# Kernel tuning notes

Measured on AMD Instinct MI355X. Metric: run time of the kernel, lower is better.

The kernel has to match this reference:

```python
import jax, jax.numpy as jnp
import numpy as np

DIM = 256
NUM_LAYERS = 64


def setup_inputs() -> dict:
    key = jax.random.key(0)
    kx, kt = jax.random.split(key)
    x = jax.random.normal(kx, (32768, DIM), dtype=jnp.float32)
    # theta[l, p]: scalar angle for pair p in layer l. Odd-offset layers use only
    # the first DIM//2 - 1 entries. Matches torch.randn(()) * pi init.
    theta = jax.random.normal(kt, (NUM_LAYERS, DIM // 2), dtype=jnp.float32) * jnp.pi
    return {"x": x, "theta": theta}


def _apply_layer(x, th, offset):
    """Apply one layer of 2x2 Givens-like rotations to pairs (i, i+1).

    U = [[c, s], [s, -c]] with c=cos(2*theta), s=sin(2*theta); U is symmetric so
    out = vec @ U.T = vec @ U -> yi = c*xi + s*xj, yj = s*xi - c*xj.
    """
    b, d = x.shape
    if offset == 0:
        npairs = d // 2
        c = jnp.cos(2.0 * th[:npairs])  # [npairs]
        s = jnp.sin(2.0 * th[:npairs])
        v = x.reshape(b, npairs, 2)
        xi, xj = v[..., 0], v[..., 1]
        yi = c * xi + s * xj
        yj = s * xi - c * xj
        return jnp.stack([yi, yj], axis=-1).reshape(b, d)
    else:
        npairs = d // 2 - 1
        c = jnp.cos(2.0 * th[:npairs])
        s = jnp.sin(2.0 * th[:npairs])
        inner = x[:, 1:d - 1].reshape(b, npairs, 2)
        xi, xj = inner[..., 0], inner[..., 1]
        yi = c * xi + s * xj
        yj = s * xi - c * xj
        mid = jnp.stack([yi, yj], axis=-1).reshape(b, d - 2)
        return jnp.concatenate([x[:, :1], mid, x[:, d - 1:]], axis=1)


def reference(x, theta):
    # Python loop over num_layers (fixed, small structural set).
    for depth in range(NUM_LAYERS):
        x = _apply_layer(x, theta[depth], depth % 2)
    return x
```

## Files before the change

### kernel.cpp

```cpp
#include <hip/hip_runtime.h>
#include <math.h>

#define DIM 256
#define NLAYERS 64

typedef __attribute__((ext_vector_type(8))) short short8;
typedef __attribute__((ext_vector_type(4))) float f32x4;

__device__ __forceinline__ float dpp_shl1_zero(float v) {
    int r = __builtin_amdgcn_update_dpp(0, __float_as_int(v), 0x130, 0xF, 0xF, true);
    return __int_as_float(r);
}
__device__ __forceinline__ float dpp_shr1_keep(float oldv, float v) {
    int r = __builtin_amdgcn_update_dpp(__float_as_int(oldv), __float_as_int(v), 0x138, 0xF, 0xF, false);
    return __int_as_float(r);
}
__device__ __forceinline__ unsigned short f2bf(float f) {
    unsigned u = __float_as_uint(f);
    u += 0x7FFFu + ((u >> 16) & 1u);
    return (unsigned short)(u >> 16);
}
__device__ __forceinline__ unsigned cvtpk_bf16(float a, float b) {
    unsigned r;
    asm("v_cvt_pk_bf16_f32 %0, %1, %2" : "=v"(r) : "v"(a), "v"(b));
    return r;
}

__global__ __launch_bounds__(256)
void build_m_kernel(const float* __restrict__ theta, unsigned short* __restrict__ bfrag) {
    __shared__ float tbl[NLAYERS * DIM];
    const int tid = threadIdx.x;
    #pragma unroll 4
    for (int kk = 0; kk < 32; ++kk) {
        int idx = tid + 256 * kk;
        int l = idx >> 7, p = idx & 127;
        float a = 2.0f * theta[idx];
        float s = __sinf(a), c = __cosf(a);
        if ((l & 1) && (p == 127)) { c = 1.0f; s = 0.0f; }
        tbl[idx * 2 + 0] = c;
        tbl[idx * 2 + 1] = s;
    }
    __syncthreads();

    const int w = tid >> 6;
    const int t = tid & 63;
    const int row = blockIdx.x * 4 + w;

    float e[4];
    #pragma unroll
    for (int j = 0; j < 4; ++j) e[j] = (4 * t + j == row) ? 1.0f : 0.0f;

    const float4* tbl4 = (const float4*)tbl;
    #pragma unroll 2
    for (int l = 0; l < NLAYERS; l += 2) {
        float4 cs = tbl4[(l << 6) + t];
        {
            float a0 = e[0], a1 = e[1], a2 = e[2], a3 = e[3];
            e[0] = cs.x * a0 + cs.y * a1;
            e[1] = cs.y * a0 - cs.x * a1;
            e[2] = cs.z * a2 + cs.w * a3;
            e[3] = cs.w * a2 - cs.z * a3;
        }
        float4 cs1 = tbl4[((l + 1) << 6) + t];
        {
            float a1 = e[1], a2 = e[2], a3 = e[3];
            float n1 = cs1.x * a1 + cs1.y * a2;
            float n2 = cs1.y * a1 - cs1.x * a2;
            float xjn = dpp_shl1_zero(e[0]);
            float n3  = cs1.z * a3 + cs1.w * xjn;
            float snd = cs1.w * a3 - cs1.z * xjn;
            e[0] = dpp_shr1_keep(e[0], snd);
            e[1] = n1; e[2] = n2; e[3] = n3;
        }
    }

    const int kt = row >> 5, g8 = (row >> 3) & 3, ki = row & 7;
    #pragma unroll
    for (int j = 0; j < 4; ++j) {
        int col = 4 * t + j;
        bfrag[(((col >> 4) * 8 + kt) * 64 + g8 * 16 + (col & 15)) * 8 + ki] = f2bf(e[j]);
    }
}

__global__ __launch_bounds__(512, 4)
void clements_gemm(const float* __restrict__ x,
                   const unsigned short* __restrict__ bfrag,
                   float* __restrict__ out) {
    __shared__ unsigned short abf[2][4096];

    const int tid = threadIdx.x;
    const int w   = tid >> 6;
    const int t   = tid & 63;
    const int l16 = t & 15;
    const int g   = t >> 4;
    const long rowbase = (long)blockIdx.x * 64;

    const int sr = tid >> 5;
    const int so = tid & 31;
    const int wsw = (((so >> 2) * 1024) + ((so & 3) * 256) + (sr * 16)) ^ ((so & 7) << 4);
    const float* const xp = x + (rowbase + sr) * 256 + so * 8;

    f32x4 pa[2], pb[2];
#define LOADR(i) { pa[(i) & 1] = *(const f32x4*)(xp + (i) * 16 * 256);       \
                   pb[(i) & 1] = *(const f32x4*)(xp + (i) * 16 * 256 + 4); }
#define CVTW(i) { union { short8 s; unsigned u[4]; } h;                      \
        h.u[0] = cvtpk_bf16(pa[(i) & 1][0], pa[(i) & 1][1]);                 \
        h.u[1] = cvtpk_bf16(pa[(i) & 1][2], pa[(i) & 1][3]);                 \
        h.u[2] = cvtpk_bf16(pb[(i) & 1][0], pb[(i) & 1][1]);                 \
        h.u[3] = cvtpk_bf16(pb[(i) & 1][2], pb[(i) & 1][3]);                 \
        *(short8*)((char*)&abf[(i) & 1][0] + wsw) = h.s; }
#define BAR() { asm volatile("s_waitcnt lgkmcnt(0)" ::: "memory");           \
                __builtin_amdgcn_s_barrier();                                \
                __builtin_amdgcn_sched_barrier(0); }

    short8 Bf[8][2];
    {
        const short8* bp = (const short8*)bfrag;
        #pragma unroll
        for (int nt = 0; nt < 2; ++nt)
            #pragma unroll
            for (int kt = 0; kt < 8; ++kt)
                Bf[kt][nt] = bp[((w * 2 + nt) * 8 + kt) * 64 + t];
    }

    auto compute = [&](int i) {
        f32x4 a0 = {0.f,0.f,0.f,0.f}, a1 = {0.f,0.f,0.f,0.f};
        const char* rb = (const char*)&abf[i & 1][0];
        #pragma unroll
        for (int kt = 0; kt < 8; ++kt) {
            short8 A = *(const short8*)(rb +
                ((kt * 1024 + t * 16) ^ (((kt * 4 + g) & 7) << 4)));
            a0 = __builtin_amdgcn_mfma_f32_16x16x32_bf16(A, Bf[kt][0], a0, 0, 0, 0);
            a1 = __builtin_amdgcn_mfma_f32_16x16x32_bf16(A, Bf[kt][1], a1, 0, 0, 0);
        }
        float* o = out + (rowbase + i * 16 + g * 4) * 256 + 32 * w + l16;
        #pragma unroll
        for (int j = 0; j < 4; ++j) {
            o[(long)j * 256 +  0] = a0[j];
            o[(long)j * 256 + 16] = a1[j];
        }
    };

    LOADR(0) LOADR(1)
    CVTW(0)
    BAR()

    #pragma unroll
    for (int c = 0; c < 4; ++c) {
        if (c + 2 < 4) LOADR(c + 2)
        compute(c);
        if (c + 1 < 4) {
            CVTW(c + 1)
            BAR()
        }
    }
#undef LOADR
#undef CVTW
#undef BAR
}

__global__ __launch_bounds__(1024, 4)
void clements_direct(const float* __restrict__ x,
                     const float* __restrict__ theta,
                     float* __restrict__ out) {
    __shared__ float tbl[NLAYERS * DIM];
    const int tid = threadIdx.x;
    #pragma unroll
    for (int k = 0; k < 8; ++k) {
        int idx = tid + 1024 * k;
        int l = idx >> 7;
        int p = idx & 127;
        float s, c;
        sincosf(2.0f * theta[idx], &s, &c);
        if ((l & 1) && (p == 127)) { c = 1.0f; s = 0.0f; }
        tbl[idx * 2 + 0] = c;
        tbl[idx * 2 + 1] = s;
    }
    __syncthreads();
    const int w = tid >> 6;
    const int t = tid & 63;
    const long base = ((long)blockIdx.x * 16 + w) * 8;
    float e[8][4];
    #pragma unroll
    for (int r = 0; r < 8; ++r) {
        float4 v = ((const float4*)(x + (base + r) * (long)DIM))[t];
        e[r][0] = v.x; e[r][1] = v.y; e[r][2] = v.z; e[r][3] = v.w;
    }
    const float4* tbl4 = (const float4*)tbl;
    #pragma unroll 2
    for (int l = 0; l < NLAYERS; l += 2) {
        float4 cs = tbl4[(l << 6) + t];
        #pragma unroll
        for (int r = 0; r < 8; ++r) {
            float a0 = e[r][0], a1 = e[r][1], a2 = e[r][2], a3 = e[r][3];
            e[r][0] = cs.x * a0 + cs.y * a1;
            e[r][1] = cs.y * a0 - cs.x * a1;
            e[r][2] = cs.z * a2 + cs.w * a3;
            e[r][3] = cs.w * a2 - cs.z * a3;
        }
        float4 cs1 = tbl4[((l + 1) << 6) + t];
        #pragma unroll
        for (int r = 0; r < 8; ++r) {
            float a1 = e[r][1], a2 = e[r][2], a3 = e[r][3];
            float n1 = cs1.x * a1 + cs1.y * a2;
            float n2 = cs1.y * a1 - cs1.x * a2;
            float xjn = dpp_shl1_zero(e[r][0]);
            float n3  = cs1.z * a3 + cs1.w * xjn;
            float snd = cs1.w * a3 - cs1.z * xjn;
            e[r][0] = dpp_shr1_keep(e[r][0], snd);
            e[r][1] = n1; e[r][2] = n2; e[r][3] = n3;
        }
    }
    #pragma unroll
    for (int r = 0; r < 8; ++r) {
        float4 v;
        v.x = e[r][0]; v.y = e[r][1]; v.z = e[r][2]; v.w = e[r][3];
        ((float4*)(out + (base + r) * (long)DIM))[t] = v;
    }
}

extern "C" void kernel_launch(void* const* d_in, const int* in_sizes, int n_in,
                              void* d_out, int out_size, void* d_ws, size_t ws_size,
                              hipStream_t stream) {
    const float* x     = (const float*)d_in[0];
    const float* theta = (const float*)d_in[1];
    float* out = (float*)d_out;

    const size_t need = (size_t)DIM * DIM * sizeof(unsigned short);
    if (ws_size >= need) {
        unsigned short* bfrag = (unsigned short*)d_ws;
        hipLaunchKernelGGL(build_m_kernel, dim3(64),  dim3(256), 0, stream, theta, bfrag);
        hipLaunchKernelGGL(clements_gemm,  dim3(512), dim3(512), 0, stream, x, bfrag, out);
    } else {
        hipLaunchKernelGGL(clements_direct, dim3(256), dim3(1024), 0, stream, x, theta, out);
    }
}
```

Before: 24.04 us.

## Split GEMM output columns across two 256-thread blocks and hoist x prefetch

The GEMM kernel now uses 256-thread blocks, each covering one 64-row slab and half of the 256 output columns, so the grid doubles to 1024 blocks. Each thread loads and converts two rows of x per stage, and the first x prefetches are issued before the B-fragment register loads to overlap their latency. The trade-off is that every x row slab is now read and converted to bf16 twice, once by each column-half block, which doubles x read traffic in exchange for more, smaller blocks and better latency hiding.

```diff
diff --git a/kernel.cpp b/kernel.cpp
--- a/kernel.cpp
+++ b/kernel.cpp
@@ -82,7 +82,7 @@
     }
 }
 
-__global__ __launch_bounds__(512, 4)
+__global__ __launch_bounds__(256, 4)
 void clements_gemm(const float* __restrict__ x,
                    const unsigned short* __restrict__ bfrag,
                    float* __restrict__ out) {
@@ -93,35 +93,52 @@
     const int t   = tid & 63;
     const int l16 = t & 15;
     const int g   = t >> 4;
-    const long rowbase = (long)blockIdx.x * 64;
-
-    const int sr = tid >> 5;
-    const int so = tid & 31;
-    const int wsw = (((so >> 2) * 1024) + ((so & 3) * 256) + (sr * 16)) ^ ((so & 7) << 4);
-    const float* const xp = x + (rowbase + sr) * 256 + so * 8;
-
-    f32x4 pa[2], pb[2];
-#define LOADR(i) { pa[(i) & 1] = *(const f32x4*)(xp + (i) * 16 * 256);       \
-                   pb[(i) & 1] = *(const f32x4*)(xp + (i) * 16 * 256 + 4); }
-#define CVTW(i) { union { short8 s; unsigned u[4]; } h;                      \
-        h.u[0] = cvtpk_bf16(pa[(i) & 1][0], pa[(i) & 1][1]);                 \
-        h.u[1] = cvtpk_bf16(pa[(i) & 1][2], pa[(i) & 1][3]);                 \
-        h.u[2] = cvtpk_bf16(pb[(i) & 1][0], pb[(i) & 1][1]);                 \
-        h.u[3] = cvtpk_bf16(pb[(i) & 1][2], pb[(i) & 1][3]);                 \
-        *(short8*)((char*)&abf[(i) & 1][0] + wsw) = h.s; }
-#define BAR() { asm volatile("s_waitcnt lgkmcnt(0)" ::: "memory");           \
-                __builtin_amdgcn_s_barrier();                                \
+    const int colbase = (blockIdx.x & 1) * 128 + w * 32;
+    const long rowbase = (long)(blockIdx.x >> 1) * 64;
+
+    const int o   = tid & 31;
+    const int sr2 = tid >> 5;
+    const int wsw0 = (((o >> 2) * 1024) + ((o & 3) * 256) + (sr2 * 16)) ^ ((o & 7) << 4);
+    const int wsw1 = wsw0 + 128;
+    const float* const xp = x + (rowbase + sr2) * 256 + o * 8;
+
+    f32x4 pa[2][2], pb[2][2];
+#define LOADR(i) { \
+    pa[(i) & 1][0] = *(const f32x4*)(xp + (i) * 16 * 256); \
+    pb[(i) & 1][0] = *(const f32x4*)(xp + (i) * 16 * 256 + 4); \
+    pa[(i) & 1][1] = *(const f32x4*)(xp + (i) * 16 * 256 + 8 * 256); \
+    pb[(i) & 1][1] = *(const f32x4*)(xp + (i) * 16 * 256 + 8 * 256 + 4); }
+#define CVTW(i) { \
+    union { short8 s; unsigned u[4]; } h0, h1; \
+    h0.u[0] = cvtpk_bf16(pa[(i) & 1][0][0], pa[(i) & 1][0][1]); \
+    h0.u[1] = cvtpk_bf16(pa[(i) & 1][0][2], pa[(i) & 1][0][3]); \
+    h0.u[2] = cvtpk_bf16(pb[(i) & 1][0][0], pb[(i) & 1][0][1]); \
+    h0.u[3] = cvtpk_bf16(pb[(i) & 1][0][2], pb[(i) & 1][0][3]); \
+    h1.u[0] = cvtpk_bf16(pa[(i) & 1][1][0], pa[(i) & 1][1][1]); \
+    h1.u[1] = cvtpk_bf16(pa[(i) & 1][1][2], pa[(i) & 1][1][3]); \
+    h1.u[2] = cvtpk_bf16(pb[(i) & 1][1][0], pb[(i) & 1][1][1]); \
+    h1.u[3] = cvtpk_bf16(pb[(i) & 1][1][2], pb[(i) & 1][1][3]); \
+    *(short8*)((char*)&abf[(i) & 1][0] + wsw0) = h0.s; \
+    *(short8*)((char*)&abf[(i) & 1][0] + wsw1) = h1.s; }
+#define BAR() { asm volatile("s_waitcnt lgkmcnt(0)" ::: "memory"); \
+                __builtin_amdgcn_s_barrier(); \
                 __builtin_amdgcn_sched_barrier(0); }
+
+    LOADR(0) LOADR(1)
 
     short8 Bf[8][2];
     {
         const short8* bp = (const short8*)bfrag;
+        const int cb16 = (blockIdx.x & 1) * 8 + w * 2;
         #pragma unroll
         for (int nt = 0; nt < 2; ++nt)
             #pragma unroll
             for (int kt = 0; kt < 8; ++kt)
-                Bf[kt][nt] = bp[((w * 2 + nt) * 8 + kt) * 64 + t];
-    }
+                Bf[kt][nt] = bp[((cb16 + nt) * 8 + kt) * 64 + t];
+    }
+
+    CVTW(0)
+    BAR()
 
     auto compute = [&](int i) {
         f32x4 a0 = {0.f,0.f,0.f,0.f}, a1 = {0.f,0.f,0.f,0.f};
@@ -133,17 +150,13 @@
             a0 = __builtin_amdgcn_mfma_f32_16x16x32_bf16(A, Bf[kt][0], a0, 0, 0, 0);
             a1 = __builtin_amdgcn_mfma_f32_16x16x32_bf16(A, Bf[kt][1], a1, 0, 0, 0);
         }
-        float* o = out + (rowbase + i * 16 + g * 4) * 256 + 32 * w + l16;
+        float* op = out + (rowbase + i * 16 + g * 4) * 256 + colbase + l16;
         #pragma unroll
         for (int j = 0; j < 4; ++j) {
-            o[(long)j * 256 +  0] = a0[j];
-            o[(long)j * 256 + 16] = a1[j];
+            op[(long)j * 256 +  0] = a0[j];
+            op[(long)j * 256 + 16] = a1[j];
         }
     };
-
-    LOADR(0) LOADR(1)
-    CVTW(0)
-    BAR()
 
     #pragma unroll
     for (int c = 0; c < 4; ++c) {
@@ -229,8 +242,8 @@
     const size_t need = (size_t)DIM * DIM * sizeof(unsigned short);
     if (ws_size >= need) {
         unsigned short* bfrag = (unsigned short*)d_ws;
-        hipLaunchKernelGGL(build_m_kernel, dim3(64),  dim3(256), 0, stream, theta, bfrag);
-        hipLaunchKernelGGL(clements_gemm,  dim3(512), dim3(512), 0, stream, x, bfrag, out);
+        hipLaunchKernelGGL(build_m_kernel, dim3(64),   dim3(256), 0, stream, theta, bfrag);
+        hipLaunchKernelGGL(clements_gemm,  dim3(1024), dim3(256), 0, stream, x, bfrag, out);
     } else {
         hipLaunchKernelGGL(clements_direct, dim3(256), dim3(1024), 0, stream, x, theta, out);
     }
```

New measurement: 27.41 us. 14.0% more time.
